# Optimization experiments

Hardware: AMD Instinct MI355X
Metric: run time of the kernel (lower is better)

The kernel has to match this reference:

```python
import jax, jax.numpy as jnp
import numpy as np

FD, FO, FK, H = 1024, 512, 128, 4
N = 32768


def setup_inputs() -> dict:
    key = jax.random.key(0)
    ks = jax.random.split(key, 8)
    s = 0.02
    return {
        "Xd": jax.random.normal(ks[0], (N, FD), dtype=jnp.float32),
        "Xo": jax.random.normal(ks[1], (N, FO), dtype=jnp.float32),
        "Wq": jax.random.normal(ks[2], (FO, FK * H), dtype=jnp.float32) * s,
        "bq": jnp.zeros((FK * H,), dtype=jnp.float32),
        "Wk": jax.random.normal(ks[3], (FD, FK * H), dtype=jnp.float32) * s,
        "bk": jnp.zeros((FK * H,), dtype=jnp.float32),
        "Wv": jax.random.normal(ks[4], (FD, FD * H), dtype=jnp.float32) * s,
        "bv": jnp.zeros((FD * H,), dtype=jnp.float32),
    }


def reference(Xd, Xo, Wq, bq, Wk, bk, Wv, bv):
    n = Xd.shape[0]
    Q = (Xo @ Wq + bq).reshape(n, H, FK)      # (n, H, fk)
    K = (Xd @ Wk + bk).reshape(n, H, FK)      # (n, H, fk)
    V = (Xd @ Wv + bv).reshape(n, H, FD)      # (n, H, fd)
    scores = jnp.sum(Q * K, axis=2, keepdims=True)  # (n, H, 1), no softmax
    Z = scores * V                              # (n, H, fd)
    Z = jnp.max(Z, axis=1)                      # max pooling over heads -> (n, fd)
    return Z  # dropout is identity in inference
```

## Files before the change

### kernel.cpp

```cpp
#include <hip/hip_runtime.h>

typedef __attribute__((ext_vector_type(8))) short short8;
typedef __attribute__((ext_vector_type(4))) float f32x4;

#define GLL16(gp, lp) __builtin_amdgcn_global_load_lds( \
    (__attribute__((address_space(1))) void*)(gp), \
    (__attribute__((address_space(3))) void*)(lp), 16, 0, 0)

__device__ __forceinline__ unsigned short f2b(float f) {
  unsigned int u = __builtin_bit_cast(unsigned int, f);
  u += 0x7fffu + ((u >> 16) & 1u);
  return (unsigned short)(u >> 16);
}
__device__ __forceinline__ float b2f(unsigned short s) {
  unsigned int u = ((unsigned int)s) << 16;
  return __builtin_bit_cast(float, u);
}

__global__ __launch_bounds__(256) void conv_k(const float* __restrict__ in,
                                              short8* __restrict__ out, long n8) {
  for (long i = (long)blockIdx.x * 256 + threadIdx.x; i < n8;
       i += (long)gridDim.x * 256) {
    const float4* p = (const float4*)in + 2 * i;
    float4 a = p[0], b = p[1];
    short8 v;
    v[0] = (short)f2b(a.x); v[1] = (short)f2b(a.y);
    v[2] = (short)f2b(a.z); v[3] = (short)f2b(a.w);
    v[4] = (short)f2b(b.x); v[5] = (short)f2b(b.y);
    v[6] = (short)f2b(b.z); v[7] = (short)f2b(b.w);
    out[i] = v;
  }
}

__global__ __launch_bounds__(256) void tconv_k(const float* __restrict__ in,
                                               unsigned short* __restrict__ out,
                                               int K, int C, int inter) {
  __shared__ float t[32][33];
  int k0 = blockIdx.x * 32, c0 = blockIdx.y * 32;
  int tx = threadIdx.x & 31, ty = threadIdx.x >> 5;
#pragma unroll
  for (int p = 0; p < 4; ++p)
    t[ty + p * 8][tx] = in[(size_t)(k0 + ty + p * 8) * C + c0 + tx];
  __syncthreads();
#pragma unroll
  for (int p = 0; p < 4; ++p) {
    int c = ty + p * 8;
    int gc = c0 + c;
    int orow = inter ? ((gc & 1023) * 4 + (gc >> 10)) : gc;
    out[(size_t)orow * K + k0 + tx] = f2b(t[tx][c]);
  }
}

template <int KD>
__global__ __launch_bounds__(512, 2) void gemm_v256_k(
    const unsigned short* __restrict__ A, const unsigned short* __restrict__ Bt,
    const float* __restrict__ bias, const float* __restrict__ sc,
    float* __restrict__ Z) {
  __shared__ __align__(16) unsigned short Ash[2][16384];
  __shared__ __align__(16) unsigned short Bsh[2][16384];
  __shared__ float s_sc[1024];

  int tid = threadIdx.x;
  int bid = blockIdx.x;
  int cpx = gridDim.x >> 3;
  int lb = (bid & 7) * cpx + (bid >> 3);
  int mtile = lb >> 4, nt0 = lb & 15;
  long m0 = (long)mtile * 256;
  int l = tid & 63, wid = tid >> 6, wm = wid >> 2, wn = wid & 3;

  for (int i = tid; i < 1024; i += 512) s_sc[i] = sc[m0 * 4 + i];

  int rowg = tid >> 3;
  int srcOff = rowg * (KD * 2) + (((tid & 7) ^ (rowg & 7)) << 4);
  const char* aB = (const char*)(A + m0 * KD) + srcOff;
  const char* bB = (const char*)(Bt + (long)nt0 * 256 * KD) + srcOff;
  char* AshB = (char*)Ash;
  char* BshB = (char*)Bsh;
  int dstOff = wid * 1024;

  auto stage = [&](int k, int bb) {
#pragma unroll
    for (int h = 0; h < 2; ++h)
#pragma unroll
      for (int s = 0; s < 2; ++s) {
        int go = (h * 128 + s * 64) * (KD * 2) + k * 128;
        int lo = bb * 32768 + h * 16384 + s * 8192 + dstOff;
        GLL16(aB + go, AshB + lo);
        GLL16(bB + go, BshB + lo);
      }
  };

  f32x4 zero = {0.f, 0.f, 0.f, 0.f};
  f32x4 acc[8][4];
#pragma unroll
  for (int m = 0; m < 8; ++m)
#pragma unroll
    for (int n = 0; n < 4; ++n) acc[m][n] = zero;

  stage(0, 0);

  const int NKT = KD / 64;
  for (int kt = 0; kt < NKT; ++kt) {
    int b = kt & 1;
    asm volatile("s_waitcnt vmcnt(0)" ::: "memory");
    __builtin_amdgcn_s_barrier();
    __builtin_amdgcn_sched_barrier(0);
    if (kt + 1 < NKT) stage(kt + 1, b ^ 1);

    const char* Al = AshB + b * 32768;
    const char* Bl = BshB + b * 32768;
    int ar = l & 15;
    int kc = l >> 4;
    short8 bf[2][4], af[4];
#pragma unroll
    for (int ks = 0; ks < 2; ++ks) {
#pragma unroll
      for (int mh = 0; mh < 2; ++mh) {
        if (mh == 0) {
#pragma unroll
          for (int n = 0; n < 4; ++n) {
            int row = wn * 64 + n * 16 + ar;
            int c = (ks * 4 + kc) ^ (row & 7);
            bf[ks][n] = *(const short8*)(Bl + row * 128 + (c << 4));
          }
        }
#pragma unroll
        for (int m = 0; m < 4; ++m) {
          int row = wm * 128 + mh * 64 + m * 16 + ar;
          int c = (ks * 4 + kc) ^ (row & 7);
          af[m] = *(const short8*)(Al + row * 128 + (c << 4));
        }
        __builtin_amdgcn_s_barrier();
        __builtin_amdgcn_s_setprio(1);
#pragma unroll
        for (int m = 0; m < 4; ++m)
#pragma unroll
          for (int n = 0; n < 4; ++n)
            acc[mh * 4 + m][n] = __builtin_amdgcn_mfma_f32_16x16x32_bf16(
                af[m], bf[ks][n], acc[mh * 4 + m][n], 0, 0, 0);
        __builtin_amdgcn_s_setprio(0);
        __builtin_amdgcn_s_barrier();
      }
    }
  }

  __syncthreads();
  float* Zs = (float*)AshB;
#pragma unroll
  for (int n = 0; n < 4; ++n) {
    int pl = wn * 64 + n * 16 + (l & 15);
    int pg = nt0 * 256 + pl;
    int h = pl & 3;
    float bb = bias[(pg & 3) * 1024 + (pg >> 2)];
#pragma unroll
    for (int mi = 0; mi < 8; ++mi) {
      int rl = wm * 128 + mi * 16 + ((l >> 4) << 2);
#pragma unroll
      for (int r = 0; r < 4; ++r) {
        float z = s_sc[(rl + r) * 4 + h] * (acc[mi][n][r] + bb);
        z = fmaxf(z, __shfl_xor(z, 1));
        z = fmaxf(z, __shfl_xor(z, 2));
        if ((l & 3) == 0) Zs[(rl + r) * 64 + (pl >> 2)] = z;
      }
    }
  }
  __syncthreads();
#pragma unroll
  for (int it = 0; it < 8; ++it) {
    int i = it * 512 + tid;
    int row = i >> 4, d4 = i & 15;
    f32x4 v = *(const f32x4*)&Zs[row * 64 + d4 * 4];
    *(f32x4*)&Z[(m0 + row) * 1024 + nt0 * 64 + d4 * 4] = v;
  }
}

template <int KD, int EPI>
__global__ __launch_bounds__(256) void gemm_k(
    const unsigned short* __restrict__ A, const unsigned short* __restrict__ Bt,
    const float* __restrict__ bias, const unsigned short* __restrict__ Qb,
    unsigned short* __restrict__ outb, float* __restrict__ sc) {
  __shared__ __align__(16) unsigned short As[128 * 64];
  __shared__ __align__(16) unsigned short Bs[128 * 64];
  __shared__ float sred[128][2];

  int tid = threadIdx.x;
  int bid = blockIdx.x;
  int ntile = bid & 3, mtile = bid >> 2;
  int l = tid & 63, wid = tid >> 6, wm = wid >> 1, wn = wid & 1;
  int m0 = mtile * 128;

  const unsigned short* Ab = A + (size_t)m0 * KD;
  const unsigned short* Bb = Bt + (size_t)ntile * 128 * KD;

  f32x4 zero = {0.f, 0.f, 0.f, 0.f};
  f32x4 acc[4][4];
#pragma unroll
  for (int m = 0; m < 4; ++m)
#pragma unroll
    for (int n = 0; n < 4; ++n) acc[m][n] = zero;

  for (int kt = 0; kt < KD / 64; ++kt) {
    const unsigned short* sA = Ab + kt * 64;
    const unsigned short* sB = Bb + kt * 64;
#pragma unroll
    for (int p = 0; p < 4; ++p) {
      int row = p * 32 + wid * 8 + (l >> 3);
      int sch = (l & 7) ^ (row & 7);
      GLL16((const char*)(sA + (size_t)row * KD) + sch * 16,
            (char*)As + p * 4096 + wid * 1024);
    }
#pragma unroll
    for (int p = 0; p < 4; ++p) {
      int row = p * 32 + wid * 8 + (l >> 3);
      int sch = (l & 7) ^ (row & 7);
      GLL16((const char*)(sB + (size_t)row * KD) + sch * 16,
            (char*)Bs + p * 4096 + wid * 1024);
    }
    __syncthreads();
#pragma unroll
    for (int ks = 0; ks < 2; ++ks) {
      short8 af[4], bfr[4];
#pragma unroll
      for (int m = 0; m < 4; ++m) {
        int row = wm * 64 + m * 16 + (l & 15);
        int kc = ks * 4 + (l >> 4);
        af[m] = *(const short8*)((const char*)As + row * 128 +
                                 ((kc ^ (row & 7)) << 4));
      }
#pragma unroll
      for (int n = 0; n < 4; ++n) {
        int row = wn * 64 + n * 16 + (l & 15);
        int kc = ks * 4 + (l >> 4);
        bfr[n] = *(const short8*)((const char*)Bs + row * 128 +
                                  ((kc ^ (row & 7)) << 4));
      }
#pragma unroll
      for (int m = 0; m < 4; ++m)
#pragma unroll
        for (int n = 0; n < 4; ++n)
          acc[m][n] = __builtin_amdgcn_mfma_f32_16x16x32_bf16(af[m], bfr[n],
                                                              acc[m][n], 0, 0, 0);
    }
    __syncthreads();
  }

  if constexpr (EPI == 0) {
#pragma unroll
    for (int n = 0; n < 4; ++n) {
      int col = ntile * 128 + wn * 64 + n * 16 + (l & 15);
      float bb = bias[col];
#pragma unroll
      for (int m = 0; m < 4; ++m) {
        int rowb = m0 + wm * 64 + m * 16 + ((l >> 4) << 2);
#pragma unroll
        for (int r = 0; r < 4; ++r)
          outb[(size_t)(rowb + r) * 512 + col] = f2b(acc[m][n][r] + bb);
      }
    }
  } else {
    float part[4][4] = {};
#pragma unroll
    for (int n = 0; n < 4; ++n) {
      int col = ntile * 128 + wn * 64 + n * 16 + (l & 15);
      float bb = bias[col];
#pragma unroll
      for (int m = 0; m < 4; ++m) {
        int rowb = m0 + wm * 64 + m * 16 + ((l >> 4) << 2);
#pragma unroll
        for (int r = 0; r < 4; ++r) {
          float kv = acc[m][n][r] + bb;
          part[m][r] += kv * b2f(Qb[(size_t)(rowb + r) * 512 + col]);
        }
      }
    }
#pragma unroll
    for (int m = 0; m < 4; ++m)
#pragma unroll
      for (int r = 0; r < 4; ++r) {
        float s = part[m][r];
        s += __shfl_xor(s, 1);
        s += __shfl_xor(s, 2);
        s += __shfl_xor(s, 4);
        s += __shfl_xor(s, 8);
        if ((l & 15) == 0)
          sred[wm * 64 + m * 16 + ((l >> 4) << 2) + r][wn] = s;
      }
    __syncthreads();
    if (tid < 128) sc[(size_t)(m0 + tid) * 4 + ntile] = sred[tid][0] + sred[tid][1];
  }
}

__global__ __launch_bounds__(256) void naive_k(
    const float* __restrict__ Xd, const float* __restrict__ Xo,
    const float* __restrict__ Wq, const float* __restrict__ bq,
    const float* __restrict__ Wk, const float* __restrict__ bk,
    const float* __restrict__ Wv, const float* __restrict__ bv,
    float* __restrict__ Z) {
  int i = blockIdx.x, t = threadIdx.x;
  __shared__ float xd[1024], xo[512], s[4];
  for (int j = t; j < 1024; j += 256) xd[j] = Xd[(size_t)i * 1024 + j];
  for (int j = t; j < 512; j += 256) xo[j] = Xo[(size_t)i * 512 + j];
  if (t < 4) s[t] = 0.f;
  __syncthreads();
  for (int c = t; c < 512; c += 256) {
    float q = bq[c], k = bk[c];
    for (int j = 0; j < 512; ++j) q += xo[j] * Wq[(size_t)j * 512 + c];
    for (int j = 0; j < 1024; ++j) k += xd[j] * Wk[(size_t)j * 512 + c];
    atomicAdd(&s[c >> 7], q * k);
  }
  __syncthreads();
  for (int d = t; d < 1024; d += 256) {
    float z = -INFINITY;
    for (int h = 0; h < 4; ++h) {
      float v = bv[h * 1024 + d];
      for (int j = 0; j < 1024; ++j) v += xd[j] * Wv[(size_t)j * 4096 + h * 1024 + d];
      z = fmaxf(z, s[h] * v);
    }
    Z[(size_t)i * 1024 + d] = z;
  }
}

extern "C" void kernel_launch(void* const* d_in, const int* in_sizes, int n_in,
                              void* d_out, int out_size, void* d_ws, size_t ws_size,
                              hipStream_t stream) {
  const float* Xd = (const float*)d_in[0];
  const float* Xo = (const float*)d_in[1];
  const float* Wq = (const float*)d_in[2];
  const float* bq = (const float*)d_in[3];
  const float* Wk = (const float*)d_in[4];
  const float* bk = (const float*)d_in[5];
  const float* Wv = (const float*)d_in[6];
  const float* bv = (const float*)d_in[7];
  float* Z = (float*)d_out;
  long N = in_sizes[0] / 1024;

  size_t sz_Xd = (size_t)N * 1024 * 2, sz_Xo = (size_t)N * 512 * 2;
  size_t sz_Wq = (size_t)512 * 512 * 2, sz_Wk = (size_t)512 * 1024 * 2;
  size_t sz_Wv = (size_t)4096 * 1024 * 2;
  size_t sz_Qb = (size_t)N * 512 * 2, sz_sc = (size_t)N * 4 * 4;
  size_t o_Xo = sz_Xd, o_Wq = o_Xo + sz_Xo, o_Wk = o_Wq + sz_Wq,
         o_Wv = o_Wk + sz_Wk, o_Qb = o_Wv + sz_Wv, o_sc = o_Qb + sz_Qb;
  size_t need = o_sc + sz_sc;

  if (ws_size < need || (N % 256) != 0) {
    naive_k<<<(int)N, 256, 0, stream>>>(Xd, Xo, Wq, bq, Wk, bk, Wv, bv, Z);
    return;
  }

  char* w = (char*)d_ws;
  unsigned short* Xd_b = (unsigned short*)w;
  unsigned short* Xo_b = (unsigned short*)(w + o_Xo);
  unsigned short* Wq_t = (unsigned short*)(w + o_Wq);
  unsigned short* Wk_t = (unsigned short*)(w + o_Wk);
  unsigned short* Wv_p = (unsigned short*)(w + o_Wv);
  unsigned short* Qb   = (unsigned short*)(w + o_Qb);
  float* sc = (float*)(w + o_sc);

  conv_k<<<2048, 256, 0, stream>>>(Xd, (short8*)Xd_b, N * 1024 / 8);
  conv_k<<<2048, 256, 0, stream>>>(Xo, (short8*)Xo_b, N * 512 / 8);
  tconv_k<<<dim3(16, 16), 256, 0, stream>>>(Wq, Wq_t, 512, 512, 0);
  tconv_k<<<dim3(32, 16), 256, 0, stream>>>(Wk, Wk_t, 1024, 512, 0);
  tconv_k<<<dim3(32, 128), 256, 0, stream>>>(Wv, Wv_p, 1024, 4096, 1);

  int mt = (int)(N / 128);
  gemm_k<512, 0><<<mt * 4, 256, 0, stream>>>(Xo_b, Wq_t, bq, nullptr, Qb, nullptr);
  gemm_k<1024, 1><<<mt * 4, 256, 0, stream>>>(Xd_b, Wk_t, bk, Qb, nullptr, sc);
  gemm_v256_k<1024><<<(int)(N / 256) * 16, 512, 0, stream>>>(Xd_b, Wv_p, bv, sc, Z);
}
```

Measured before the change: 533.9 us.

## Deepen V-GEMM pipeline to four LDS stages with smaller K tiles

Restructures the bf16 MFMA V-projection GEMM from a double-buffered 64-wide K tile to a four-buffer ring of 32-wide K tiles, keeping three tiles of loads in flight with partial vmcnt waits. The LDS layout is repacked so two rows share a 128-byte swizzled line, and the LDS fragment offsets are precomputed once per thread. The aim is to hide global-load latency better and cut per-iteration address math. In exchange it uses 128 KB of LDS per block, which likely limits occupancy to one block per CU despite launch bounds asking for two, and it doubles the number of barrier iterations.

```diff
diff --git a/kernel.cpp b/kernel.cpp
--- a/kernel.cpp
+++ b/kernel.cpp
@@ -56,10 +56,10 @@
     const unsigned short* __restrict__ A, const unsigned short* __restrict__ Bt,
     const float* __restrict__ bias, const float* __restrict__ sc,
     float* __restrict__ Z) {
-  __shared__ __align__(16) unsigned short Ash[2][16384];
-  __shared__ __align__(16) unsigned short Bsh[2][16384];
+  __shared__ __align__(16) char lds[131072];
   __shared__ float s_sc[1024];
 
+  const int NKT = KD / 32;
   int tid = threadIdx.x;
   int bid = blockIdx.x;
   int cpx = gridDim.x >> 3;
@@ -70,25 +70,35 @@
 
   for (int i = tid; i < 1024; i += 512) s_sc[i] = sc[m0 * 4 + i];
 
-  int rowg = tid >> 3;
-  int srcOff = rowg * (KD * 2) + (((tid & 7) ^ (rowg & 7)) << 4);
-  const char* aB = (const char*)(A + m0 * KD) + srcOff;
-  const char* bB = (const char*)(Bt + (long)nt0 * 256 * KD) + srcOff;
-  char* AshB = (char*)Ash;
-  char* BshB = (char*)Bsh;
+  int srg = tid >> 3, slot = tid & 7;
+  int se = slot ^ (srg & 7);
+  int par = se >> 2, kc = se & 3;
+  int rowb = srg * 2 + par;
+  const char* aT = (const char*)(A + m0 * KD) + (long)rowb * (KD * 2) + kc * 16;
+  const char* bT = (const char*)(Bt + (long)nt0 * 256 * KD) + (long)rowb * (KD * 2) + kc * 16;
+  char* ldsb = (char*)lds;
   int dstOff = wid * 1024;
 
-  auto stage = [&](int k, int bb) {
-#pragma unroll
-    for (int h = 0; h < 2; ++h)
-#pragma unroll
-      for (int s = 0; s < 2; ++s) {
-        int go = (h * 128 + s * 64) * (KD * 2) + k * 128;
-        int lo = bb * 32768 + h * 16384 + s * 8192 + dstOff;
-        GLL16(aB + go, AshB + lo);
-        GLL16(bB + go, BshB + lo);
-      }
+  auto stage = [&](int kt, int bb) {
+    int ko = kt * 64;
+    GLL16(aT + ko,                 ldsb + bb * 32768 + dstOff);
+    GLL16(aT + 128 * (KD * 2) + ko, ldsb + bb * 32768 + 8192 + dstOff);
+    GLL16(bT + ko,                 ldsb + bb * 32768 + 16384 + dstOff);
+    GLL16(bT + 128 * (KD * 2) + ko, ldsb + bb * 32768 + 24576 + dstOff);
   };
+
+  int ar = l & 15, kcl = l >> 4;
+  int aoffR[8], boffR[4];
+#pragma unroll
+  for (int m = 0; m < 8; ++m) {
+    int wr = wm * 128 + m * 16 + ar, sr = wr >> 1;
+    aoffR[m] = sr * 128 + (((((wr & 1) << 2) | kcl) ^ (sr & 7)) << 4);
+  }
+#pragma unroll
+  for (int n = 0; n < 4; ++n) {
+    int br = wn * 64 + n * 16 + ar, sr = br >> 1;
+    boffR[n] = sr * 128 + (((((br & 1) << 2) | kcl) ^ (sr & 7)) << 4);
+  }
 
   f32x4 zero = {0.f, 0.f, 0.f, 0.f};
   f32x4 acc[8][4];
@@ -97,55 +107,52 @@
 #pragma unroll
     for (int n = 0; n < 4; ++n) acc[m][n] = zero;
 
-  stage(0, 0);
-
-  const int NKT = KD / 64;
-  for (int kt = 0; kt < NKT; ++kt) {
-    int b = kt & 1;
-    asm volatile("s_waitcnt vmcnt(0)" ::: "memory");
+  stage(0, 0); stage(1, 1); stage(2, 2);
+
+  for (int t = 0; t < NKT; ++t) {
+    if (t < NKT - 2)       asm volatile("s_waitcnt vmcnt(8)" ::: "memory");
+    else if (t == NKT - 2) asm volatile("s_waitcnt vmcnt(4)" ::: "memory");
+    else                   asm volatile("s_waitcnt vmcnt(0)" ::: "memory");
     __builtin_amdgcn_s_barrier();
     __builtin_amdgcn_sched_barrier(0);
-    if (kt + 1 < NKT) stage(kt + 1, b ^ 1);
-
-    const char* Al = AshB + b * 32768;
-    const char* Bl = BshB + b * 32768;
-    int ar = l & 15;
-    int kc = l >> 4;
-    short8 bf[2][4], af[4];
-#pragma unroll
-    for (int ks = 0; ks < 2; ++ks) {
-#pragma unroll
-      for (int mh = 0; mh < 2; ++mh) {
-        if (mh == 0) {
-#pragma unroll
-          for (int n = 0; n < 4; ++n) {
-            int row = wn * 64 + n * 16 + ar;
-            int c = (ks * 4 + kc) ^ (row & 7);
-            bf[ks][n] = *(const short8*)(Bl + row * 128 + (c << 4));
-          }
-        }
-#pragma unroll
-        for (int m = 0; m < 4; ++m) {
-          int row = wm * 128 + mh * 64 + m * 16 + ar;
-          int c = (ks * 4 + kc) ^ (row & 7);
-          af[m] = *(const short8*)(Al + row * 128 + (c << 4));
-        }
-        __builtin_amdgcn_s_barrier();
-        __builtin_amdgcn_s_setprio(1);
-#pragma unroll
-        for (int m = 0; m < 4; ++m)
-#pragma unroll
-          for (int n = 0; n < 4; ++n)
-            acc[mh * 4 + m][n] = __builtin_amdgcn_mfma_f32_16x16x32_bf16(
-                af[m], bf[ks][n], acc[mh * 4 + m][n], 0, 0, 0);
-        __builtin_amdgcn_s_setprio(0);
-        __builtin_amdgcn_s_barrier();
-      }
-    }
-  }
-
-  __syncthreads();
-  float* Zs = (float*)AshB;
+    if (t + 3 < NKT) stage(t + 3, (t + 3) & 3);
+    __builtin_amdgcn_sched_barrier(0);
+
+    const char* Al = ldsb + (t & 3) * 32768;
+    const char* Bl = Al + 16384;
+    short8 bf[4], af[4], af2[4];
+#pragma unroll
+    for (int n = 0; n < 4; ++n) bf[n] = *(const short8*)(Bl + boffR[n]);
+#pragma unroll
+    for (int m = 0; m < 4; ++m) af[m] = *(const short8*)(Al + aoffR[m]);
+#pragma unroll
+    for (int m = 0; m < 4; ++m) af2[m] = *(const short8*)(Al + aoffR[4 + m]);
+
+    __builtin_amdgcn_s_barrier();
+    __builtin_amdgcn_sched_barrier(0);
+    __builtin_amdgcn_s_setprio(1);
+#pragma unroll
+    for (int m = 0; m < 4; ++m)
+#pragma unroll
+      for (int n = 0; n < 4; ++n)
+        acc[m][n] = __builtin_amdgcn_mfma_f32_16x16x32_bf16(af[m], bf[n],
+                                                            acc[m][n], 0, 0, 0);
+    __builtin_amdgcn_s_setprio(0);
+
+    __builtin_amdgcn_s_barrier();
+    __builtin_amdgcn_sched_barrier(0);
+    __builtin_amdgcn_s_setprio(1);
+#pragma unroll
+    for (int m = 0; m < 4; ++m)
+#pragma unroll
+      for (int n = 0; n < 4; ++n)
+        acc[4 + m][n] = __builtin_amdgcn_mfma_f32_16x16x32_bf16(af2[m], bf[n],
+                                                                acc[4 + m][n], 0, 0, 0);
+    __builtin_amdgcn_s_setprio(0);
+  }
+
+  __syncthreads();
+  float* Zs = (float*)ldsb;
 #pragma unroll
   for (int n = 0; n < 4; ++n) {
     int pl = wn * 64 + n * 16 + (l & 15);
```

Result: slower. 561.5 us (+5.2%).
